# Kernel optimization log

Measured on AMD Instinct MI355X. Metric: run time of the kernel, lower is better.

## Reference

```python
import jax, jax.numpy as jnp
import numpy as np

STUDENT_FRAMES = [0, 2, 4, 6]
EXTRA_FRAMES = [1, 3, 5, 7]       # teacher-only frames, sorted
SHARED_T = [2, 4, 6]              # shared frames in teacher indexing
SHARED_S = [1, 2, 3]              # same frames in student indexing
TOPK = 4
EPS = 1e-8                        # eps of _cos_angle's F.normalize
HUBER_DELTA = 1.0
A1 = A2 = A3 = 1.0


def _huber(pred, target, delta=HUBER_DELTA):
    err = pred - target
    ae = jnp.abs(err)
    return jnp.where(ae <= delta, 0.5 * err * err, delta * (ae - 0.5 * delta))


def _angles(h, r, c):
    """Cosine angles for the triangle (shared=h [B,F,S,D], ref=r [B,R,D], sim=c [B,R,K,D]).
    Expands cos(a-b, c-b) via pairwise dot products so no [.,.,.,.,D] tensor is materialized.
    Returns (a1, a2, a3) each of shape [B,F,R,S,K]."""
    ss = jnp.einsum('bfsd,brkd->bfrsk', h, c)   # shared . sim
    sr = jnp.einsum('bfsd,brd->bfrs', h, r)     # shared . ref
    rk = jnp.einsum('brd,brkd->brk', r, c)      # ref . sim
    rr = jnp.sum(r * r, -1)                     # [B,R]
    kk = jnp.sum(c * c, -1)                     # [B,R,K]
    hh = jnp.sum(h * h, -1)                     # [B,F,S]
    sr_ = sr[..., None]                         # bfrs1
    rk_ = rk[:, None, :, None, :]               # b1r1k
    rr_ = rr[:, None, :, None, None]            # b1r11
    kk_ = kk[:, None, :, None, :]               # b1r1k
    hh_ = hh[:, :, None, :, None]               # bf1s1
    n_hr = jnp.sqrt(jnp.maximum(hh_ + rr_ - 2.0 * sr_, 0.0))  # ||shared-ref||
    n_cr = jnp.sqrt(jnp.maximum(kk_ + rr_ - 2.0 * rk_, 0.0))  # ||sim-ref||
    n_hc = jnp.sqrt(jnp.maximum(hh_ + kk_ - 2.0 * ss, 0.0))   # ||shared-sim||
    def cos(num, na, nb):
        return num / (jnp.maximum(na, EPS) * jnp.maximum(nb, EPS))
    a1 = cos(ss - sr_ - rk_ + rr_, n_hr, n_cr)  # cos(shared-ref, sim-ref)
    a2 = cos(sr_ - rk_ - ss + kk_, n_cr, n_hc)  # cos(ref-sim, shared-sim)
    a3 = cos(rk_ - sr_ - ss + hh_, n_hr, n_hc)  # cos(ref-shared, sim-shared)
    return a1, a2, a3


def setup_inputs() -> dict:
    key = jax.random.key(0)
    k1, k2, k3, k4 = jax.random.split(key, 4)
    B, V, P, D = 4, 8, 1369, 2048
    teacher_feats = jax.random.normal(k1, (B, V, P, D), jnp.float32)
    student_feats = jax.random.normal(k2, (B, len(STUDENT_FRAMES), P, D), jnp.float32)
    ref_perm = jax.random.permutation(k3, P)[:128].astype(jnp.int32)
    shared_perm = jax.random.permutation(k4, P)[:128].astype(jnp.int32)
    return {'teacher_feats': teacher_feats, 'student_feats': student_feats,
            'ref_perm': ref_perm, 'shared_perm': shared_perm}


def reference(teacher_feats, student_feats, ref_perm, shared_perm):
    teacher = jax.lax.stop_gradient(teacher_feats)  # teacher side is fully detached
    B, V, P, D = teacher.shape

    ref_t = teacher[:, STUDENT_FRAMES[0], ref_perm, :]        # [B,R,D]
    ref_s = student_feats[:, 0, ref_perm, :]                  # [B,R,D]

    # extra (teacher-only) frames concatenated along patches -> [B, 4*P, D]
    extra_t = teacher[:, jnp.array(EXTRA_FRAMES)].reshape(B, len(EXTRA_FRAMES) * P, D)

    # cosine similarity + topk selection (selection_mode='topk')
    ref_tn = ref_t / jnp.maximum(jnp.linalg.norm(ref_t, axis=-1, keepdims=True), 1e-12)
    extra_tn = extra_t / jnp.maximum(jnp.linalg.norm(extra_t, axis=-1, keepdims=True), 1e-12)
    sim = jnp.einsum('brd,bed->bre', ref_tn, extra_tn)        # [B,R,4P]
    _, idx = jax.lax.top_k(sim, TOPK)                         # [B,R,K]
    sim_high = jax.vmap(lambda e, i: e[i])(extra_t, idx)      # [B,R,K,D]

    shared_t = teacher[:, jnp.array(SHARED_T)][:, :, shared_perm, :]        # [B,F,S,D]
    shared_s = student_feats[:, jnp.array(SHARED_S)][:, :, shared_perm, :]  # [B,F,S,D]

    a1_t, a2_t, a3_t = _angles(shared_t, ref_t, sim_high)
    a1_s, a2_s, a3_s = _angles(shared_s, ref_s, sim_high)

    l1 = _huber(a1_s, a1_t).mean()
    l2 = _huber(a2_s, a2_t).mean()
    l3 = _huber(a3_s, a3_t).mean()
    loss = A1 * l1 + A2 * l2 + A3 * l3
    return loss
```

## Files before the change

### kernel.cpp

```cpp
#include <hip/hip_runtime.h>
#include <hip/hip_bf16.h>

#define B_ 4
#define V_ 8
#define P_ 1369
#define D_ 2048
#define R_ 128
#define F_ 3
#define K_ 4
#define E_ 5476
#define CAND_ 8
#define EPS_ 1e-8f
#define ETILES_ 86
#define SIMBLK_ (ETILES_*B_*2)
#define HOFF_ ((size_t)B_*384*640)

typedef unsigned short u16;
typedef __attribute__((ext_vector_type(8))) short bf16x8;
typedef __attribute__((ext_vector_type(4))) float f32x4;

__device__ inline int pack2bf(float lo, float hi){
  __hip_bfloat162 h = __float22bfloat162_rn(make_float2(lo, hi));
  int r; __builtin_memcpy(&r, &h, 4); return r;
}
__device__ inline float sq8(float4 a, float4 b){
  return a.x*a.x + a.y*a.y + a.z*a.z + a.w*a.w
       + b.x*b.x + b.y*b.y + b.z*b.z + b.w*b.w;
}
__device__ inline float huber1(float e){
  float ae = fabsf(e);
  return ae <= 1.0f ? 0.5f*e*e : (ae - 0.5f);
}
__device__ inline float blk_sum(float v, float* scr){
  for (int off = 32; off; off >>= 1) v += __shfl_xor(v, off, 64);
  __syncthreads();
  if ((threadIdx.x & 63) == 0) scr[threadIdx.x >> 6] = v;
  __syncthreads();
  float s = scr[0] + scr[1] + scr[2] + scr[3];
  __syncthreads();
  return s;
}

__global__ __launch_bounds__(256) void k_prep_ref(
    const float* __restrict__ teacher, const float* __restrict__ student,
    const int* __restrict__ ref_perm,
    u16* __restrict__ ref_tn, float* __restrict__ rr_t, float* __restrict__ rr_s){
  __shared__ float scr[4];
  int br = blockIdx.x, b = br >> 7, r = br & 127, t = threadIdx.x;
  int p = ref_perm[r];
  const float* tp = teacher + ((size_t)(b*V_)*P_ + p)*D_;
  const float* sp = student + ((size_t)(b*4)*P_ + p)*D_;
  float4 x0 = *(const float4*)(tp + t*8);
  float4 x1 = *(const float4*)(tp + t*8 + 4);
  float sumt = blk_sum(sq8(x0, x1), scr);
  float4 y0 = *(const float4*)(sp + t*8);
  float4 y1 = *(const float4*)(sp + t*8 + 4);
  float sums = blk_sum(sq8(y0, y1), scr);
  if (t == 0){ rr_t[br] = sumt; rr_s[br] = sums; }
  float inv = 1.0f / fmaxf(sqrtf(sumt), 1e-12f);
  int4 pt = { pack2bf(x0.x*inv, x0.y*inv), pack2bf(x0.z*inv, x0.w*inv),
              pack2bf(x1.x*inv, x1.y*inv), pack2bf(x1.z*inv, x1.w*inv) };
  *(int4*)(ref_tn + (size_t)br*D_ + t*8) = pt;
}

__global__ __launch_bounds__(256) void k_sim_fused(
    const float* __restrict__ teacher, const float* __restrict__ student,
    const u16* __restrict__ ref_tn, const int* __restrict__ shared_perm,
    float* __restrict__ simPart, float* __restrict__ nsqPart,
    u16* __restrict__ shT, u16* __restrict__ shS,
    float* __restrict__ hhT, float* __restrict__ hhS){
  __shared__ __align__(16) u16 As[128][72];
  __shared__ __align__(16) u16 Bs[64][72];
  __shared__ float scr4[4];
  int bx = blockIdx.x, t = threadIdx.x;
  if (bx < SIMBLK_){
    int h = bx / (ETILES_*B_);
    int rem = bx % (ETILES_*B_);
    int b = rem / ETILES_, et = rem % ETILES_;
    int e0 = et * 64;
    int lane = t & 63, w = t >> 6, wm = w >> 1, wn = w & 1;
    f32x4 acc[4][2];
    for (int i = 0; i < 4; i++)
      for (int j = 0; j < 2; j++)
        acc[i][j] = (f32x4){0.f, 0.f, 0.f, 0.f};
    int arow = t >> 1, acol = (t & 1) * 32;
    int brow = t >> 2, bcol = (t & 3) * 16;
    int e = e0 + brow;
    const u16* asrc = ref_tn + ((size_t)(b*128 + arow))*D_ + acol;
    const float* bsrc = nullptr;
    if (e < E_) bsrc = teacher + ((size_t)(b*V_ + 1 + 2*(e / P_))*P_ + (e % P_))*D_ + bcol;
    float q = 0.0f;
    int lr = lane & 15;
    int kbeg = h * 1024, kend = kbeg + 1024;
    int4 aa0, aa1, aa2, aa3;
    float4 za0, za1, za2, za3;
    {
      aa0 = *(const int4*)(asrc + kbeg);      aa1 = *(const int4*)(asrc + kbeg + 8);
      aa2 = *(const int4*)(asrc + kbeg + 16); aa3 = *(const int4*)(asrc + kbeg + 24);
      if (bsrc){
        za0 = *(const float4*)(bsrc + kbeg);      za1 = *(const float4*)(bsrc + kbeg + 4);
        za2 = *(const float4*)(bsrc + kbeg + 8);  za3 = *(const float4*)(bsrc + kbeg + 12);
      } else { za0 = make_float4(0.f,0.f,0.f,0.f); za1 = za0; za2 = za0; za3 = za0; }
    }
    for (int k0 = kbeg; k0 < kend; k0 += 64){
      __syncthreads();
      *(int4*)&As[arow][acol]      = aa0;
      *(int4*)&As[arow][acol + 8]  = aa1;
      *(int4*)&As[arow][acol + 16] = aa2;
      *(int4*)&As[arow][acol + 24] = aa3;
      q += sq8(za0, za1) + sq8(za2, za3);
      int4 p0 = { pack2bf(za0.x, za0.y), pack2bf(za0.z, za0.w),
                  pack2bf(za1.x, za1.y), pack2bf(za1.z, za1.w) };
      int4 p1 = { pack2bf(za2.x, za2.y), pack2bf(za2.z, za2.w),
                  pack2bf(za3.x, za3.y), pack2bf(za3.z, za3.w) };
      *(int4*)&Bs[brow][bcol]     = p0;
      *(int4*)&Bs[brow][bcol + 8] = p1;
      __syncthreads();
      int kn = k0 + 64;
      if (kn < kend){
        aa0 = *(const int4*)(asrc + kn);      aa1 = *(const int4*)(asrc + kn + 8);
        aa2 = *(const int4*)(asrc + kn + 16); aa3 = *(const int4*)(asrc + kn + 24);
        if (bsrc){
          za0 = *(const float4*)(bsrc + kn);      za1 = *(const float4*)(bsrc + kn + 4);
          za2 = *(const float4*)(bsrc + kn + 8);  za3 = *(const float4*)(bsrc + kn + 12);
        }
      }
#pragma unroll
      for (int kk = 0; kk < 2; kk++){
        int kof = kk*32 + (lane >> 4) * 8;
        bf16x8 bf0 = *(const bf16x8*)&Bs[wn*32 + lr][kof];
        bf16x8 bf1 = *(const bf16x8*)&Bs[wn*32 + 16 + lr][kof];
#pragma unroll
        for (int mi = 0; mi < 4; mi++){
          bf16x8 af = *(const bf16x8*)&As[wm*64 + mi*16 + lr][kof];
          acc[mi][0] = __builtin_amdgcn_mfma_f32_16x16x32_bf16(af, bf0, acc[mi][0], 0, 0, 0);
          acc[mi][1] = __builtin_amdgcn_mfma_f32_16x16x32_bf16(af, bf1, acc[mi][1], 0, 0, 0);
        }
      }
    }
    q += __shfl_xor(q, 1, 64);
    q += __shfl_xor(q, 2, 64);
    if ((t & 3) == 0 && e < E_) nsqPart[(size_t)(h*4 + b)*E_ + e] = q;
    int lg = lane >> 4;
#pragma unroll
    for (int mi = 0; mi < 4; mi++){
#pragma unroll
      for (int ni = 0; ni < 2; ni++){
        int el = wn*32 + ni*16 + lr;
        int e_idx = e0 + el;
        if (e_idx < E_){
#pragma unroll
          for (int reg = 0; reg < 4; reg++){
            int r_idx = wm*64 + mi*16 + lg*4 + reg;
            simPart[((size_t)((h*4 + b)*128 + r_idx))*E_ + e_idx] = acc[mi][ni][reg];
          }
        }
      }
    }
  } else {
    int id = bx - SIMBLK_;
    int b = id / 384, fs = id % 384;
    int f = fs >> 7, s = fs & 127;
    int p = shared_perm[s];
    const float* tp = teacher + ((size_t)(b*V_ + 2 + 2*f)*P_ + p)*D_;
    const float* sp = student + ((size_t)(b*4 + 1 + f)*P_ + p)*D_;
    float4 x0 = *(const float4*)(tp + t*8);
    float4 x1 = *(const float4*)(tp + t*8 + 4);
    float sumt = blk_sum(sq8(x0, x1), scr4);
    int4 pt = { pack2bf(x0.x, x0.y), pack2bf(x0.z, x0.w),
                pack2bf(x1.x, x1.y), pack2bf(x1.z, x1.w) };
    *(int4*)(shT + (size_t)id*D_ + t*8) = pt;
    float4 y0 = *(const float4*)(sp + t*8);
    float4 y1 = *(const float4*)(sp + t*8 + 4);
    float sums = blk_sum(sq8(y0, y1), scr4);
    int4 ps = { pack2bf(y0.x, y0.y), pack2bf(y0.z, y0.w),
                pack2bf(y1.x, y1.y), pack2bf(y1.z, y1.w) };
    *(int4*)(shS + (size_t)id*D_ + t*8) = ps;
    if (t == 0){ hhT[id] = sumt; hhS[id] = sums; }
  }
}

__global__ __launch_bounds__(256) void k_rescore(
    const float* __restrict__ teacher, const float* __restrict__ student,
    const int* __restrict__ ref_perm,
    const float* __restrict__ simPart, const float* __restrict__ nsqPart,
    const float* __restrict__ rr_t,
    u16* __restrict__ packT, u16* __restrict__ packS,
    float* __restrict__ kkw, float* __restrict__ rkT, float* __restrict__ rkS){
  __shared__ float v[E_];
  __shared__ float rT[D_];
  __shared__ float rS[D_];
  __shared__ float tv[256];
  __shared__ int   ti[256];
  __shared__ float rv[4];
  __shared__ int ri[4];
  __shared__ int cand[CAND_];
  __shared__ float csim[CAND_], cq[CAND_], cdT[CAND_];
  __shared__ int order[4];
  int br = blockIdx.x, b = br >> 7, r = br & 127, t = threadIdx.x;
  int lane = t & 63, w = t >> 6;
  const float* p0 = simPart + ((size_t)(b*128 + r))*E_;
  const float* p1 = simPart + ((size_t)((4 + b)*128 + r))*E_;
  const float* q0 = nsqPart + (size_t)b*E_;
  const float* q1 = nsqPart + (size_t)(4 + b)*E_;
  for (int i = t; i < E_; i += 256){
    float qq = q0[i] + q1[i];
    float inv = 1.0f / fmaxf(sqrtf(qq), 1e-12f);
    v[i] = (p0[i] + p1[i]) * inv;
  }
  __syncthreads();
  {
    float bv = -3.4e38f; int bi = 0x7fffffff;
    for (int i = t; i < E_; i += 256){
      float x = v[i];
      if (x > bv){ bv = x; bi = i; }
    }
    tv[t] = bv; ti[t] = bi;
  }
  __syncthreads();
  for (int c = 0; c < CAND_; c++){
    float mv = tv[t]; int mi2 = ti[t];
    for (int off = 32; off; off >>= 1){
      float ov = __shfl_down(mv, off, 64);
      int   oi = __shfl_down(mi2, off, 64);
      if (ov > mv || (ov == mv && oi < mi2)){ mv = ov; mi2 = oi; }
    }
    if (lane == 0){ rv[w] = mv; ri[w] = mi2; }
    __syncthreads();
    if (t == 0){
      for (int w2 = 1; w2 < 4; w2++)
        if (rv[w2] > rv[0] || (rv[w2] == rv[0] && ri[w2] < ri[0])){ rv[0] = rv[w2]; ri[0] = ri[w2]; }
      cand[c] = ri[0];
      v[ri[0]] = -3.4e38f;
    }
    __syncthreads();
    int win = cand[c];
    if (t == (win & 255)){
      float nb = -3.4e38f; int nbi = 0x7fffffff;
      for (int i = t; i < E_; i += 256){
        float x = v[i];
        if (x > nb){ nb = x; nbi = i; }
      }
      tv[t] = nb; ti[t] = nbi;
    }
    __syncthreads();
  }
  int p = ref_perm[r];
  const float* tp = teacher + ((size_t)(b*V_)*P_ + p)*D_;
  const float* sp = student + ((size_t)(b*4)*P_ + p)*D_;
  float4 x0 = *(const float4*)(tp + t*8);
  float4 x1 = *(const float4*)(tp + t*8 + 4);
  float4 y0 = *(const float4*)(sp + t*8);
  float4 y1 = *(const float4*)(sp + t*8 + 4);
  *(float4*)&rT[t*8]   = x0; *(float4*)&rT[t*8+4] = x1;
  *(float4*)&rS[t*8]   = y0; *(float4*)&rS[t*8+4] = y1;
  {
    int4 pt = { pack2bf(x0.x, x0.y), pack2bf(x0.z, x0.w),
                pack2bf(x1.x, x1.y), pack2bf(x1.z, x1.w) };
    *(int4*)(packT + ((size_t)(br*5 + 4))*D_ + t*8) = pt;
    int4 ps = { pack2bf(y0.x, y0.y), pack2bf(y0.z, y0.w),
                pack2bf(y1.x, y1.y), pack2bf(y1.z, y1.w) };
    *(int4*)(packS + ((size_t)(br*5 + 4))*D_ + t*8) = ps;
  }
  float invt = 1.0f / fmaxf(sqrtf(rr_t[br]), 1e-12f);
  __syncthreads();
  for (int c = w; c < CAND_; c += 4){
    int e = cand[c];
    const float* xp = teacher + ((size_t)(b*V_ + 1 + 2*(e / P_))*P_ + (e % P_))*D_;
    float d = 0.f, q = 0.f;
#pragma unroll
    for (int j = 0; j < 32; j++){
      float xv = xp[lane + 64*j];
      d += xv * rT[lane + 64*j];
      q += xv * xv;
    }
    for (int off = 32; off; off >>= 1){
      d += __shfl_xor(d, off, 64);
      q += __shfl_xor(q, off, 64);
    }
    if (lane == 0){
      cdT[c] = d; cq[c] = q;
      csim[c] = d * invt / fmaxf(sqrtf(q), 1e-12f);
    }
  }
  __syncthreads();
  if (t == 0){
    unsigned used = 0;
    for (int k = 0; k < 4; k++){
      int best = -1;
      for (int c = 0; c < CAND_; c++){
        if (used & (1u << c)) continue;
        if (best < 0){ best = c; continue; }
        if (csim[c] > csim[best] ||
            (csim[c] == csim[best] && cand[c] < cand[best])) best = c;
      }
      used |= 1u << best;
      order[k] = best;
    }
  }
  __syncthreads();
  {
    int c = order[w];
    int e = cand[c];
    const float* xp = teacher + ((size_t)(b*V_ + 1 + 2*(e / P_))*P_ + (e % P_))*D_;
    float ds = 0.f;
#pragma unroll
    for (int j = 0; j < 32; j++)
      ds += xp[lane + 64*j] * rS[lane + 64*j];
    for (int off = 32; off; off >>= 1) ds += __shfl_xor(ds, off, 64);
    if (lane == 0){
      kkw[br*4 + w] = cq[c];
      rkT[br*4 + w] = cdT[c];
      rkS[br*4 + w] = ds;
    }
    const float* src = xp + lane*32;
#pragma unroll
    for (int u = 0; u < 4; u++){
      float4 a  = *(const float4*)(src + u*8);
      float4 b2 = *(const float4*)(src + u*8 + 4);
      int4 pc = { pack2bf(a.x, a.y), pack2bf(a.z, a.w),
                  pack2bf(b2.x, b2.y), pack2bf(b2.z, b2.w) };
      size_t po = ((size_t)(br*5 + w))*D_ + lane*32 + u*8;
      *(int4*)(packT + po) = pc;
      *(int4*)(packS + po) = pc;
    }
  }
}

__global__ __launch_bounds__(256) void k_angle_gemm(
    const u16* __restrict__ shT, const u16* __restrict__ shS,
    const u16* __restrict__ packT, const u16* __restrict__ packS,
    float* __restrict__ outT, float* __restrict__ outS){
  __shared__ __align__(16) u16 As[128][72];
  __shared__ __align__(16) u16 Bs[64][72];
  int which = blockIdx.z >> 1, h = blockIdx.z & 1;
  const u16* A  = which ? shS : shT;
  const u16* Bp = which ? packS : packT;
  float* out = (which ? outS : outT) + h * HOFF_;
  int b = blockIdx.y;
  int mt = blockIdx.x % 3, nt = blockIdx.x / 3;
  int m0 = mt*128, n0 = nt*64;
  int t = threadIdx.x, lane = t & 63, w = t >> 6, wm = w >> 1, wn = w & 1;
  f32x4 acc[4][2];
  for (int i = 0; i < 4; i++)
    for (int j = 0; j < 2; j++)
      acc[i][j] = (f32x4){0.f, 0.f, 0.f, 0.f};
  int arow = t >> 1, acol = (t & 1) * 32;
  int brow = t >> 2, bcol = (t & 3) * 16;
  const u16* asrc = A  + ((size_t)(b*384 + m0 + arow))*D_ + acol;
  const u16* bsrc = Bp + ((size_t)(b*640 + n0 + brow))*D_ + bcol;
  int lr = lane & 15;
  int kbeg = h * 1024, kend = kbeg + 1024;
  int4 ra0, ra1, ra2, ra3, rb0, rb1;
  ra0 = *(const int4*)(asrc + kbeg);      ra1 = *(const int4*)(asrc + kbeg + 8);
  ra2 = *(const int4*)(asrc + kbeg + 16); ra3 = *(const int4*)(asrc + kbeg + 24);
  rb0 = *(const int4*)(bsrc + kbeg);      rb1 = *(const int4*)(bsrc + kbeg + 8);
  for (int k0 = kbeg; k0 < kend; k0 += 64){
    __syncthreads();
    *(int4*)&As[arow][acol]      = ra0;
    *(int4*)&As[arow][acol + 8]  = ra1;
    *(int4*)&As[arow][acol + 16] = ra2;
    *(int4*)&As[arow][acol + 24] = ra3;
    *(int4*)&Bs[brow][bcol]     = rb0;
    *(int4*)&Bs[brow][bcol + 8] = rb1;
    __syncthreads();
    int kn = k0 + 64;
    if (kn < kend){
      ra0 = *(const int4*)(asrc + kn);      ra1 = *(const int4*)(asrc + kn + 8);
      ra2 = *(const int4*)(asrc + kn + 16); ra3 = *(const int4*)(asrc + kn + 24);
      rb0 = *(const int4*)(bsrc + kn);      rb1 = *(const int4*)(bsrc + kn + 8);
    }
#pragma unroll
    for (int kk = 0; kk < 2; kk++){
      int kof = kk*32 + (lane >> 4) * 8;
      bf16x8 bf0 = *(const bf16x8*)&Bs[wn*32 + lr][kof];
      bf16x8 bf1 = *(const bf16x8*)&Bs[wn*32 + 16 + lr][kof];
#pragma unroll
      for (int mi = 0; mi < 4; mi++){
        bf16x8 af = *(const bf16x8*)&As[wm*64 + mi*16 + lr][kof];
        acc[mi][0] = __builtin_amdgcn_mfma_f32_16x16x32_bf16(af, bf0, acc[mi][0], 0, 0, 0);
        acc[mi][1] = __builtin_amdgcn_mfma_f32_16x16x32_bf16(af, bf1, acc[mi][1], 0, 0, 0);
      }
    }
  }
  int lg = lane >> 4;
#pragma unroll
  for (int mi = 0; mi < 4; mi++)
#pragma unroll
    for (int ni = 0; ni < 2; ni++)
#pragma unroll
      for (int reg = 0; reg < 4; reg++){
        int r_idx = wm*64 + mi*16 + lg*4 + reg;
        int c_idx = wn*32 + ni*16 + lr;
        out[((size_t)(b*384 + m0 + r_idx))*640 + n0 + c_idx] = acc[mi][ni][reg];
      }
}

__global__ __launch_bounds__(256) void k_assemble(
    const float* __restrict__ outT, const float* __restrict__ outS,
    const float* __restrict__ hhT, const float* __restrict__ hhS,
    const float* __restrict__ rrT, const float* __restrict__ rrS,
    const float* __restrict__ kkw, const float* __restrict__ rkT, const float* __restrict__ rkS,
    double* __restrict__ partials){
  __shared__ double dscr[4];
  int idx = blockIdx.x*256 + threadIdx.x;
  int r = idx & 127, s = (idx >> 7) & 127, bf = idx >> 14;
  int f = bf % 3, b = bf / 3;
  int fs = f*128 + s;
  size_t base = ((size_t)(b*384 + fs))*640 + r*5;
  const float* oT0 = outT + base; const float* oT1 = oT0 + HOFF_;
  const float* oS0 = outS + base; const float* oS1 = oS0 + HOFF_;
  float hh_t = hhT[b*384 + fs], hh_s = hhS[b*384 + fs];
  float rr_tv = rrT[b*128 + r], rr_sv = rrS[b*128 + r];
  float sr_t = oT0[4] + oT1[4], sr_s = oS0[4] + oS1[4];
  float nhr_t = sqrtf(fmaxf(hh_t + rr_tv - 2.0f*sr_t, 0.0f));
  float nhr_s = sqrtf(fmaxf(hh_s + rr_sv - 2.0f*sr_s, 0.0f));
  float h1 = 0.f, h2 = 0.f, h3 = 0.f;
#pragma unroll
  for (int k = 0; k < 4; k++){
    float ss_t = oT0[k] + oT1[k], ss_s = oS0[k] + oS1[k];
    float kk = kkw[(b*128 + r)*4 + k];
    float rk_t = rkT[(b*128 + r)*4 + k];
    float rk_s = rkS[(b*128 + r)*4 + k];
    float ncr_t = sqrtf(fmaxf(kk + rr_tv - 2.0f*rk_t, 0.0f));
    float ncr_s = sqrtf(fmaxf(kk + rr_sv - 2.0f*rk_s, 0.0f));
    float nhc_t = sqrtf(fmaxf(hh_t + kk - 2.0f*ss_t, 0.0f));
    float nhc_s = sqrtf(fmaxf(hh_s + kk - 2.0f*ss_s, 0.0f));
    float a1t = (ss_t - sr_t - rk_t + rr_tv) / (fmaxf(nhr_t, EPS_) * fmaxf(ncr_t, EPS_));
    float a2t = (sr_t - rk_t - ss_t + kk)    / (fmaxf(ncr_t, EPS_) * fmaxf(nhc_t, EPS_));
    float a3t = (rk_t - sr_t - ss_t + hh_t)  / (fmaxf(nhr_t, EPS_) * fmaxf(nhc_t, EPS_));
    float a1s = (ss_s - sr_s - rk_s + rr_sv) / (fmaxf(nhr_s, EPS_) * fmaxf(ncr_s, EPS_));
    float a2s = (sr_s - rk_s - ss_s + kk)    / (fmaxf(ncr_s, EPS_) * fmaxf(nhc_s, EPS_));
    float a3s = (rk_s - sr_s - ss_s + hh_s)  / (fmaxf(nhr_s, EPS_) * fmaxf(nhc_s, EPS_));
    h1 += huber1(a1s - a1t);
    h2 += huber1(a2s - a2t);
    h3 += huber1(a3s - a3t);
  }
  double d1 = h1, d2 = h2, d3 = h3;
  for (int off = 32; off; off >>= 1){
    d1 += __shfl_xor(d1, off, 64);
    d2 += __shfl_xor(d2, off, 64);
    d3 += __shfl_xor(d3, off, 64);
  }
  int w = threadIdx.x >> 6;
  if ((threadIdx.x & 63) == 0) dscr[w] = d1;
  __syncthreads();
  if (threadIdx.x == 0) partials[blockIdx.x*3 + 0] = dscr[0]+dscr[1]+dscr[2]+dscr[3];
  __syncthreads();
  if ((threadIdx.x & 63) == 0) dscr[w] = d2;
  __syncthreads();
  if (threadIdx.x == 0) partials[blockIdx.x*3 + 1] = dscr[0]+dscr[1]+dscr[2]+dscr[3];
  __syncthreads();
  if ((threadIdx.x & 63) == 0) dscr[w] = d3;
  __syncthreads();
  if (threadIdx.x == 0) partials[blockIdx.x*3 + 2] = dscr[0]+dscr[1]+dscr[2]+dscr[3];
}

__global__ __launch_bounds__(256) void k_final(
    const double* __restrict__ partials, float* __restrict__ out){
  __shared__ double dscr[12];
  int t = threadIdx.x;
  double l1 = 0, l2 = 0, l3 = 0;
  for (int i = t; i < 768; i += 256){
    l1 += partials[i*3 + 0];
    l2 += partials[i*3 + 1];
    l3 += partials[i*3 + 2];
  }
  for (int off = 32; off; off >>= 1){
    l1 += __shfl_xor(l1, off, 64);
    l2 += __shfl_xor(l2, off, 64);
    l3 += __shfl_xor(l3, off, 64);
  }
  int w = t >> 6;
  if ((t & 63) == 0){ dscr[w*3] = l1; dscr[w*3+1] = l2; dscr[w*3+2] = l3; }
  __syncthreads();
  if (t == 0){
    double L1 = dscr[0] + dscr[3] + dscr[6] + dscr[9];
    double L2 = dscr[1] + dscr[4] + dscr[7] + dscr[10];
    double L3 = dscr[2] + dscr[5] + dscr[8] + dscr[11];
    out[0] = (float)((L1 + L2 + L3) / 786432.0);
  }
}

extern "C" void kernel_launch(void* const* d_in, const int* in_sizes, int n_in,
                              void* d_out, int out_size, void* d_ws, size_t ws_size,
                              hipStream_t stream){
  (void)in_sizes; (void)n_in; (void)out_size; (void)ws_size;
  const float* teacher = (const float*)d_in[0];
  const float* student = (const float*)d_in[1];
  const int* ref_perm = (const int*)d_in[2];
  const int* shared_perm = (const int*)d_in[3];
  float* out = (float*)d_out;

  char* ws = (char*)d_ws;
  size_t off = 0;
  auto alloc = [&](size_t bytes)->char*{
    char* pp = ws + off;
    off += (bytes + 255) & ~(size_t)255;
    return pp;
  };
  u16*    ref_tn  = (u16*)   alloc((size_t)B_*R_*D_*sizeof(u16));
  float*  rr_t    = (float*) alloc(B_*R_*sizeof(float));
  float*  rr_s    = (float*) alloc(B_*R_*sizeof(float));
  float*  kkw     = (float*) alloc(B_*R_*K_*sizeof(float));
  float*  rkT     = (float*) alloc(B_*R_*K_*sizeof(float));
  float*  rkS     = (float*) alloc(B_*R_*K_*sizeof(float));
  u16*    shT     = (u16*)   alloc((size_t)B_*384*D_*sizeof(u16));
  u16*    shS     = (u16*)   alloc((size_t)B_*384*D_*sizeof(u16));
  float*  hhT     = (float*) alloc(B_*384*sizeof(float));
  float*  hhS     = (float*) alloc(B_*384*sizeof(float));
  float*  outT    = (float*) alloc((size_t)2*B_*384*640*sizeof(float));
  float*  outS    = (float*) alloc((size_t)2*B_*384*640*sizeof(float));
  double* partials= (double*)alloc(768*3*sizeof(double));
  float*  simPart = (float*) alloc((size_t)2*B_*R_*E_*sizeof(float));
  float*  nsqPart = (float*) alloc((size_t)2*B_*E_*sizeof(float));
  u16*    packT   = (u16*)   alloc((size_t)B_*R_*5*D_*sizeof(u16));
  u16*    packS   = (u16*)   alloc((size_t)B_*R_*5*D_*sizeof(u16));

  k_prep_ref<<<dim3(B_*R_), dim3(256), 0, stream>>>(teacher, student, ref_perm,
                                                    ref_tn, rr_t, rr_s);
  k_sim_fused<<<dim3(SIMBLK_ + 1536), dim3(256), 0, stream>>>(
      teacher, student, ref_tn, shared_perm, simPart, nsqPart, shT, shS, hhT, hhS);
  k_rescore<<<dim3(B_*R_), dim3(256), 0, stream>>>(teacher, student, ref_perm,
                                                   simPart, nsqPart, rr_t,
                                                   packT, packS, kkw, rkT, rkS);
  k_angle_gemm<<<dim3(30, B_, 4), dim3(256), 0, stream>>>(shT, shS, packT, packS, outT, outS);
  k_assemble<<<dim3(768), dim3(256), 0, stream>>>(outT, outS, hhT, hhS, rr_t, rr_s, kkw, rkT, rkS, partials);
  k_final<<<dim3(1), dim3(256), 0, stream>>>(partials, out);
}
```

Measured before the change: 126.4 us.

## Store split-K GEMM partials in bf16 and fuse final reduction via atomic counter

The split-K partial outputs of the similarity GEMM and the angle GEMM are now stored as bf16 instead of fp32. This halves the intermediate traffic between kernels. The separate final-reduction kernel is removed: the last assemble block, found through an atomic counter reset in the first kernel, sums the partials, which saves one launch. The bf16 partials lose precision, which could change top-k selection and the angle values near degeneracies.

```diff
diff --git a/kernel.cpp b/kernel.cpp
--- a/kernel.cpp
+++ b/kernel.cpp
@@ -14,11 +14,20 @@
 #define ETILES_ 86
 #define SIMBLK_ (ETILES_*B_*2)
 #define HOFF_ ((size_t)B_*384*640)
+#define NASM_ 768
 
 typedef unsigned short u16;
 typedef __attribute__((ext_vector_type(8))) short bf16x8;
 typedef __attribute__((ext_vector_type(4))) float f32x4;
 
+__device__ inline u16 f2bf(float f){
+  unsigned int u = __float_as_uint(f);
+  u = u + 0x7fffu + ((u >> 16) & 1u);
+  return (u16)(u >> 16);
+}
+__device__ inline float bf2f(u16 h){
+  return __uint_as_float((unsigned)h << 16);
+}
 __device__ inline int pack2bf(float lo, float hi){
   __hip_bfloat162 h = __float22bfloat162_rn(make_float2(lo, hi));
   int r; __builtin_memcpy(&r, &h, 4); return r;
@@ -44,9 +53,11 @@
 __global__ __launch_bounds__(256) void k_prep_ref(
     const float* __restrict__ teacher, const float* __restrict__ student,
     const int* __restrict__ ref_perm,
-    u16* __restrict__ ref_tn, float* __restrict__ rr_t, float* __restrict__ rr_s){
+    u16* __restrict__ ref_tn, float* __restrict__ rr_t, float* __restrict__ rr_s,
+    unsigned* __restrict__ cnt){
   __shared__ float scr[4];
   int br = blockIdx.x, b = br >> 7, r = br & 127, t = threadIdx.x;
+  if (br == 0 && t == 0) *cnt = 0u;
   int p = ref_perm[r];
   const float* tp = teacher + ((size_t)(b*V_)*P_ + p)*D_;
   const float* sp = student + ((size_t)(b*4)*P_ + p)*D_;
@@ -66,7 +77,7 @@
 __global__ __launch_bounds__(256) void k_sim_fused(
     const float* __restrict__ teacher, const float* __restrict__ student,
     const u16* __restrict__ ref_tn, const int* __restrict__ shared_perm,
-    float* __restrict__ simPart, float* __restrict__ nsqPart,
+    u16* __restrict__ simPart, float* __restrict__ nsqPart,
     u16* __restrict__ shT, u16* __restrict__ shS,
     float* __restrict__ hhT, float* __restrict__ hhS){
   __shared__ __align__(16) u16 As[128][72];
@@ -152,7 +163,7 @@
 #pragma unroll
           for (int reg = 0; reg < 4; reg++){
             int r_idx = wm*64 + mi*16 + lg*4 + reg;
-            simPart[((size_t)((h*4 + b)*128 + r_idx))*E_ + e_idx] = acc[mi][ni][reg];
+            simPart[((size_t)((h*4 + b)*128 + r_idx))*E_ + e_idx] = f2bf(acc[mi][ni][reg]);
           }
         }
       }
@@ -183,7 +194,7 @@
 __global__ __launch_bounds__(256) void k_rescore(
     const float* __restrict__ teacher, const float* __restrict__ student,
     const int* __restrict__ ref_perm,
-    const float* __restrict__ simPart, const float* __restrict__ nsqPart,
+    const u16* __restrict__ simPart, const float* __restrict__ nsqPart,
     const float* __restrict__ rr_t,
     u16* __restrict__ packT, u16* __restrict__ packS,
     float* __restrict__ kkw, float* __restrict__ rkT, float* __restrict__ rkS){
@@ -199,14 +210,14 @@
   __shared__ int order[4];
   int br = blockIdx.x, b = br >> 7, r = br & 127, t = threadIdx.x;
   int lane = t & 63, w = t >> 6;
-  const float* p0 = simPart + ((size_t)(b*128 + r))*E_;
-  const float* p1 = simPart + ((size_t)((4 + b)*128 + r))*E_;
+  const u16* p0 = simPart + ((size_t)(b*128 + r))*E_;
+  const u16* p1 = simPart + ((size_t)((4 + b)*128 + r))*E_;
   const float* q0 = nsqPart + (size_t)b*E_;
   const float* q1 = nsqPart + (size_t)(4 + b)*E_;
   for (int i = t; i < E_; i += 256){
     float qq = q0[i] + q1[i];
     float inv = 1.0f / fmaxf(sqrtf(qq), 1e-12f);
-    v[i] = (p0[i] + p1[i]) * inv;
+    v[i] = (bf2f(p0[i]) + bf2f(p1[i])) * inv;
   }
   __syncthreads();
   {
@@ -330,13 +341,13 @@
 __global__ __launch_bounds__(256) void k_angle_gemm(
     const u16* __restrict__ shT, const u16* __restrict__ shS,
     const u16* __restrict__ packT, const u16* __restrict__ packS,
-    float* __restrict__ outT, float* __restrict__ outS){
+    u16* __restrict__ outT, u16* __restrict__ outS){
   __shared__ __align__(16) u16 As[128][72];
   __shared__ __align__(16) u16 Bs[64][72];
   int which = blockIdx.z >> 1, h = blockIdx.z & 1;
   const u16* A  = which ? shS : shT;
   const u16* Bp = which ? packS : packT;
-  float* out = (which ? outS : outT) + h * HOFF_;
+  u16* out = (which ? outS : outT) + h * HOFF_;
   int b = blockIdx.y;
   int mt = blockIdx.x % 3, nt = blockIdx.x / 3;
   int m0 = mt*128, n0 = nt*64;
@@ -392,33 +403,36 @@
       for (int reg = 0; reg < 4; reg++){
         int r_idx = wm*64 + mi*16 + lg*4 + reg;
         int c_idx = wn*32 + ni*16 + lr;
-        out[((size_t)(b*384 + m0 + r_idx))*640 + n0 + c_idx] = acc[mi][ni][reg];
+        out[((size_t)(b*384 + m0 + r_idx))*640 + n0 + c_idx] = f2bf(acc[mi][ni][reg]);
       }
 }
 
 __global__ __launch_bounds__(256) void k_assemble(
-    const float* __restrict__ outT, const float* __restrict__ outS,
+    const u16* __restrict__ outT, const u16* __restrict__ outS,
     const float* __restrict__ hhT, const float* __restrict__ hhS,
     const float* __restrict__ rrT, const float* __restrict__ rrS,
     const float* __restrict__ kkw, const float* __restrict__ rkT, const float* __restrict__ rkS,
-    double* __restrict__ partials){
+    double* __restrict__ partials, unsigned* __restrict__ cnt, float* __restrict__ outF){
   __shared__ double dscr[4];
+  __shared__ double dfin[12];
+  __shared__ int lastFlag;
   int idx = blockIdx.x*256 + threadIdx.x;
   int r = idx & 127, s = (idx >> 7) & 127, bf = idx >> 14;
   int f = bf % 3, b = bf / 3;
   int fs = f*128 + s;
   size_t base = ((size_t)(b*384 + fs))*640 + r*5;
-  const float* oT0 = outT + base; const float* oT1 = oT0 + HOFF_;
-  const float* oS0 = outS + base; const float* oS1 = oS0 + HOFF_;
+  const u16* oT0 = outT + base; const u16* oT1 = oT0 + HOFF_;
+  const u16* oS0 = outS + base; const u16* oS1 = oS0 + HOFF_;
   float hh_t = hhT[b*384 + fs], hh_s = hhS[b*384 + fs];
   float rr_tv = rrT[b*128 + r], rr_sv = rrS[b*128 + r];
-  float sr_t = oT0[4] + oT1[4], sr_s = oS0[4] + oS1[4];
+  float sr_t = bf2f(oT0[4]) + bf2f(oT1[4]), sr_s = bf2f(oS0[4]) + bf2f(oS1[4]);
   float nhr_t = sqrtf(fmaxf(hh_t + rr_tv - 2.0f*sr_t, 0.0f));
   float nhr_s = sqrtf(fmaxf(hh_s + rr_sv - 2.0f*sr_s, 0.0f));
   float h1 = 0.f, h2 = 0.f, h3 = 0.f;
 #pragma unroll
   for (int k = 0; k < 4; k++){
-    float ss_t = oT0[k] + oT1[k], ss_s = oS0[k] + oS1[k];
+    float ss_t = bf2f(oT0[k]) + bf2f(oT1[k]);
+    float ss_s = bf2f(oS0[k]) + bf2f(oS1[k]);
     float kk = kkw[(b*128 + r)*4 + k];
     float rk_t = rkT[(b*128 + r)*4 + k];
     float rk_s = rkS[(b*128 + r)*4 + k];
@@ -453,32 +467,35 @@
   __syncthreads();
   if ((threadIdx.x & 63) == 0) dscr[w] = d3;
   __syncthreads();
-  if (threadIdx.x == 0) partials[blockIdx.x*3 + 2] = dscr[0]+dscr[1]+dscr[2]+dscr[3];
-}
-
-__global__ __launch_bounds__(256) void k_final(
-    const double* __restrict__ partials, float* __restrict__ out){
-  __shared__ double dscr[12];
-  int t = threadIdx.x;
-  double l1 = 0, l2 = 0, l3 = 0;
-  for (int i = t; i < 768; i += 256){
-    l1 += partials[i*3 + 0];
-    l2 += partials[i*3 + 1];
-    l3 += partials[i*3 + 2];
-  }
-  for (int off = 32; off; off >>= 1){
-    l1 += __shfl_xor(l1, off, 64);
-    l2 += __shfl_xor(l2, off, 64);
-    l3 += __shfl_xor(l3, off, 64);
-  }
-  int w = t >> 6;
-  if ((t & 63) == 0){ dscr[w*3] = l1; dscr[w*3+1] = l2; dscr[w*3+2] = l3; }
-  __syncthreads();
-  if (t == 0){
-    double L1 = dscr[0] + dscr[3] + dscr[6] + dscr[9];
-    double L2 = dscr[1] + dscr[4] + dscr[7] + dscr[10];
-    double L3 = dscr[2] + dscr[5] + dscr[8] + dscr[11];
-    out[0] = (float)((L1 + L2 + L3) / 786432.0);
+  if (threadIdx.x == 0){
+    partials[blockIdx.x*3 + 2] = dscr[0]+dscr[1]+dscr[2]+dscr[3];
+    __threadfence();
+    unsigned old = atomicAdd(cnt, 1u);
+    lastFlag = (old == NASM_ - 1) ? 1 : 0;
+  }
+  __syncthreads();
+  if (lastFlag){
+    __threadfence();
+    int t = threadIdx.x;
+    double l1 = 0, l2 = 0, l3 = 0;
+    for (int i = t; i < NASM_; i += 256){
+      l1 += partials[i*3 + 0];
+      l2 += partials[i*3 + 1];
+      l3 += partials[i*3 + 2];
+    }
+    for (int off = 32; off; off >>= 1){
+      l1 += __shfl_xor(l1, off, 64);
+      l2 += __shfl_xor(l2, off, 64);
+      l3 += __shfl_xor(l3, off, 64);
+    }
+    if ((t & 63) == 0){ dfin[w*3] = l1; dfin[w*3+1] = l2; dfin[w*3+2] = l3; }
+    __syncthreads();
+    if (t == 0){
+      double L1 = dfin[0] + dfin[3] + dfin[6] + dfin[9];
+      double L2 = dfin[1] + dfin[4] + dfin[7] + dfin[10];
+      double L3 = dfin[2] + dfin[5] + dfin[8] + dfin[11];
+      outF[0] = (float)((L1 + L2 + L3) / 786432.0);
+    }
   }
 }
 
@@ -509,22 +526,23 @@
   u16*    shS     = (u16*)   alloc((size_t)B_*384*D_*sizeof(u16));
   float*  hhT     = (float*) alloc(B_*384*sizeof(float));
   float*  hhS     = (float*) alloc(B_*384*sizeof(float));
-  float*  outT    = (float*) alloc((size_t)2*B_*384*640*sizeof(float));
-  float*  outS    = (float*) alloc((size_t)2*B_*384*640*sizeof(float));
-  double* partials= (double*)alloc(768*3*sizeof(double));
-  float*  simPart = (float*) alloc((size_t)2*B_*R_*E_*sizeof(float));
+  u16*    outT    = (u16*)   alloc((size_t)2*B_*384*640*sizeof(u16));
+  u16*    outS    = (u16*)   alloc((size_t)2*B_*384*640*sizeof(u16));
+  double* partials= (double*)alloc(NASM_*3*sizeof(double));
+  unsigned* cnt   = (unsigned*)alloc(256);
+  u16*    simPart = (u16*)   alloc((size_t)2*B_*R_*E_*sizeof(u16));
   float*  nsqPart = (float*) alloc((size_t)2*B_*E_*sizeof(float));
   u16*    packT   = (u16*)   alloc((size_t)B_*R_*5*D_*sizeof(u16));
   u16*    packS   = (u16*)   alloc((size_t)B_*R_*5*D_*sizeof(u16));
 
   k_prep_ref<<<dim3(B_*R_), dim3(256), 0, stream>>>(teacher, student, ref_perm,
-                                                    ref_tn, rr_t, rr_s);
+                                                    ref_tn, rr_t, rr_s, cnt);
   k_sim_fused<<<dim3(SIMBLK_ + 1536), dim3(256), 0, stream>>>(
       teacher, student, ref_tn, shared_perm, simPart, nsqPart, shT, shS, hhT, hhS);
   k_rescore<<<dim3(B_*R_), dim3(256), 0, stream>>>(teacher, student, ref_perm,
                                                    simPart, nsqPart, rr_t,
                                                    packT, packS, kkw, rkT, rkS);
   k_angle_gemm<<<dim3(30, B_, 4), dim3(256), 0, stream>>>(shT, shS, packT, packS, outT, outS);
-  k_assemble<<<dim3(768), dim3(256), 0, stream>>>(outT, outS, hhT, hhS, rr_t, rr_s, kkw, rkT, rkS, partials);
-  k_final<<<dim3(1), dim3(256), 0, stream>>>(partials, out);
-}
+  k_assemble<<<dim3(NASM_), dim3(256), 0, stream>>>(outT, outS, hhT, hhS, rr_t, rr_s,
+                                                    kkw, rkT, rkS, partials, cnt, out);
+}
```

New measurement: 132.1 us. 1.05x slower.

## Widen sim GEMM E-tile to 128 and split K three ways

Applied to the files above, without the earlier changes.

The similarity GEMM tile grows from 128x64 to 128x128 along the extra-patch dimension, so each ref_tn A tile is reused across twice as many columns and each wave issues 16 MFMAs per k-step instead of 8. The K split changes from two halves of 1024 to three chunks (704/704/640), which keeps the block count similar (516 vs 688). The rescore kernel now sums three partial sim and norm buffers. The cost is more accumulator registers and LDS per block, which may lower occupancy, plus an extra partial buffer to write and read.

```diff
diff --git a/kernel.cpp b/kernel.cpp
--- a/kernel.cpp
+++ b/kernel.cpp
@@ -11,8 +11,8 @@
 #define E_ 5476
 #define CAND_ 8
 #define EPS_ 1e-8f
-#define ETILES_ 86
-#define SIMBLK_ (ETILES_*B_*2)
+#define ETILES_ 43
+#define SIMBLK_ (ETILES_*B_*3)
 #define HOFF_ ((size_t)B_*384*640)
 
 typedef unsigned short u16;
@@ -70,51 +70,64 @@
     u16* __restrict__ shT, u16* __restrict__ shS,
     float* __restrict__ hhT, float* __restrict__ hhS){
   __shared__ __align__(16) u16 As[128][72];
-  __shared__ __align__(16) u16 Bs[64][72];
+  __shared__ __align__(16) u16 Bs[128][72];
   __shared__ float scr4[4];
   int bx = blockIdx.x, t = threadIdx.x;
   if (bx < SIMBLK_){
     int h = bx / (ETILES_*B_);
     int rem = bx % (ETILES_*B_);
     int b = rem / ETILES_, et = rem % ETILES_;
-    int e0 = et * 64;
+    int e0 = et * 128;
     int lane = t & 63, w = t >> 6, wm = w >> 1, wn = w & 1;
-    f32x4 acc[4][2];
+    f32x4 acc[4][4];
+#pragma unroll
     for (int i = 0; i < 4; i++)
-      for (int j = 0; j < 2; j++)
+#pragma unroll
+      for (int j = 0; j < 4; j++)
         acc[i][j] = (f32x4){0.f, 0.f, 0.f, 0.f};
-    int arow = t >> 1, acol = (t & 1) * 32;
-    int brow = t >> 2, bcol = (t & 3) * 16;
-    int e = e0 + brow;
-    const u16* asrc = ref_tn + ((size_t)(b*128 + arow))*D_ + acol;
+    int row = t >> 1, col32 = (t & 1) * 32;
+    int e = e0 + row;
+    const u16* asrc = ref_tn + ((size_t)(b*128 + row))*D_ + col32;
     const float* bsrc = nullptr;
-    if (e < E_) bsrc = teacher + ((size_t)(b*V_ + 1 + 2*(e / P_))*P_ + (e % P_))*D_ + bcol;
+    if (e < E_) bsrc = teacher + ((size_t)(b*V_ + 1 + 2*(e / P_))*P_ + (e % P_))*D_ + col32;
     float q = 0.0f;
     int lr = lane & 15;
-    int kbeg = h * 1024, kend = kbeg + 1024;
+    int kbeg = (h == 0) ? 0 : (h == 1 ? 704 : 1408);
+    int kend = (h == 0) ? 704 : (h == 1 ? 1408 : 2048);
     int4 aa0, aa1, aa2, aa3;
-    float4 za0, za1, za2, za3;
+    float4 za0, za1, za2, za3, za4, za5, za6, za7;
     {
       aa0 = *(const int4*)(asrc + kbeg);      aa1 = *(const int4*)(asrc + kbeg + 8);
       aa2 = *(const int4*)(asrc + kbeg + 16); aa3 = *(const int4*)(asrc + kbeg + 24);
       if (bsrc){
         za0 = *(const float4*)(bsrc + kbeg);      za1 = *(const float4*)(bsrc + kbeg + 4);
         za2 = *(const float4*)(bsrc + kbeg + 8);  za3 = *(const float4*)(bsrc + kbeg + 12);
-      } else { za0 = make_float4(0.f,0.f,0.f,0.f); za1 = za0; za2 = za0; za3 = za0; }
+        za4 = *(const float4*)(bsrc + kbeg + 16); za5 = *(const float4*)(bsrc + kbeg + 20);
+        za6 = *(const float4*)(bsrc + kbeg + 24); za7 = *(const float4*)(bsrc + kbeg + 28);
+      } else {
+        za0 = make_float4(0.f,0.f,0.f,0.f); za1 = za0; za2 = za0; za3 = za0;
+        za4 = za0; za5 = za0; za6 = za0; za7 = za0;
+      }
     }
     for (int k0 = kbeg; k0 < kend; k0 += 64){
       __syncthreads();
-      *(int4*)&As[arow][acol]      = aa0;
-      *(int4*)&As[arow][acol + 8]  = aa1;
-      *(int4*)&As[arow][acol + 16] = aa2;
-      *(int4*)&As[arow][acol + 24] = aa3;
-      q += sq8(za0, za1) + sq8(za2, za3);
+      *(int4*)&As[row][col32]      = aa0;
+      *(int4*)&As[row][col32 + 8]  = aa1;
+      *(int4*)&As[row][col32 + 16] = aa2;
+      *(int4*)&As[row][col32 + 24] = aa3;
+      q += sq8(za0, za1) + sq8(za2, za3) + sq8(za4, za5) + sq8(za6, za7);
       int4 p0 = { pack2bf(za0.x, za0.y), pack2bf(za0.z, za0.w),
                   pack2bf(za1.x, za1.y), pack2bf(za1.z, za1.w) };
       int4 p1 = { pack2bf(za2.x, za2.y), pack2bf(za2.z, za2.w),
                   pack2bf(za3.x, za3.y), pack2bf(za3.z, za3.w) };
-      *(int4*)&Bs[brow][bcol]     = p0;
-      *(int4*)&Bs[brow][bcol + 8] = p1;
+      int4 p2 = { pack2bf(za4.x, za4.y), pack2bf(za4.z, za4.w),
+                  pack2bf(za5.x, za5.y), pack2bf(za5.z, za5.w) };
+      int4 p3 = { pack2bf(za6.x, za6.y), pack2bf(za6.z, za6.w),
+                  pack2bf(za7.x, za7.y), pack2bf(za7.z, za7.w) };
+      *(int4*)&Bs[row][col32]      = p0;
+      *(int4*)&Bs[row][col32 + 8]  = p1;
+      *(int4*)&Bs[row][col32 + 16] = p2;
+      *(int4*)&Bs[row][col32 + 24] = p3;
       __syncthreads();
       int kn = k0 + 64;
       if (kn < kend){
@@ -123,30 +136,34 @@
         if (bsrc){
           za0 = *(const float4*)(bsrc + kn);      za1 = *(const float4*)(bsrc + kn + 4);
           za2 = *(const float4*)(bsrc + kn + 8);  za3 = *(const float4*)(bsrc + kn + 12);
+          za4 = *(const float4*)(bsrc + kn + 16); za5 = *(const float4*)(bsrc + kn + 20);
+          za6 = *(const float4*)(bsrc + kn + 24); za7 = *(const float4*)(bsrc + kn + 28);
         }
       }
 #pragma unroll
       for (int kk = 0; kk < 2; kk++){
         int kof = kk*32 + (lane >> 4) * 8;
-        bf16x8 bf0 = *(const bf16x8*)&Bs[wn*32 + lr][kof];
-        bf16x8 bf1 = *(const bf16x8*)&Bs[wn*32 + 16 + lr][kof];
+        bf16x8 bf[4];
+#pragma unroll
+        for (int ni = 0; ni < 4; ni++)
+          bf[ni] = *(const bf16x8*)&Bs[wn*64 + ni*16 + lr][kof];
 #pragma unroll
         for (int mi = 0; mi < 4; mi++){
           bf16x8 af = *(const bf16x8*)&As[wm*64 + mi*16 + lr][kof];
-          acc[mi][0] = __builtin_amdgcn_mfma_f32_16x16x32_bf16(af, bf0, acc[mi][0], 0, 0, 0);
-          acc[mi][1] = __builtin_amdgcn_mfma_f32_16x16x32_bf16(af, bf1, acc[mi][1], 0, 0, 0);
+#pragma unroll
+          for (int ni = 0; ni < 4; ni++)
+            acc[mi][ni] = __builtin_amdgcn_mfma_f32_16x16x32_bf16(af, bf[ni], acc[mi][ni], 0, 0, 0);
         }
       }
     }
     q += __shfl_xor(q, 1, 64);
-    q += __shfl_xor(q, 2, 64);
-    if ((t & 3) == 0 && e < E_) nsqPart[(size_t)(h*4 + b)*E_ + e] = q;
+    if ((t & 1) == 0 && e < E_) nsqPart[(size_t)(h*4 + b)*E_ + e] = q;
     int lg = lane >> 4;
 #pragma unroll
     for (int mi = 0; mi < 4; mi++){
 #pragma unroll
-      for (int ni = 0; ni < 2; ni++){
-        int el = wn*32 + ni*16 + lr;
+      for (int ni = 0; ni < 4; ni++){
+        int el = wn*64 + ni*16 + lr;
         int e_idx = e0 + el;
         if (e_idx < E_){
 #pragma unroll
@@ -201,12 +218,14 @@
   int lane = t & 63, w = t >> 6;
   const float* p0 = simPart + ((size_t)(b*128 + r))*E_;
   const float* p1 = simPart + ((size_t)((4 + b)*128 + r))*E_;
+  const float* p2 = simPart + ((size_t)((8 + b)*128 + r))*E_;
   const float* q0 = nsqPart + (size_t)b*E_;
   const float* q1 = nsqPart + (size_t)(4 + b)*E_;
+  const float* q2 = nsqPart + (size_t)(8 + b)*E_;
   for (int i = t; i < E_; i += 256){
-    float qq = q0[i] + q1[i];
+    float qq = q0[i] + q1[i] + q2[i];
     float inv = 1.0f / fmaxf(sqrtf(qq), 1e-12f);
-    v[i] = (p0[i] + p1[i]) * inv;
+    v[i] = (p0[i] + p1[i] + p2[i]) * inv;
   }
   __syncthreads();
   {
@@ -512,8 +531,8 @@
   float*  outT    = (float*) alloc((size_t)2*B_*384*640*sizeof(float));
   float*  outS    = (float*) alloc((size_t)2*B_*384*640*sizeof(float));
   double* partials= (double*)alloc(768*3*sizeof(double));
-  float*  simPart = (float*) alloc((size_t)2*B_*R_*E_*sizeof(float));
-  float*  nsqPart = (float*) alloc((size_t)2*B_*E_*sizeof(float));
+  float*  simPart = (float*) alloc((size_t)3*B_*R_*E_*sizeof(float));
+  float*  nsqPart = (float*) alloc((size_t)3*B_*E_*sizeof(float));
   u16*    packT   = (u16*)   alloc((size_t)B_*R_*5*D_*sizeof(u16));
   u16*    packS   = (u16*)   alloc((size_t)B_*R_*5*D_*sizeof(u16));
 
@@ -525,6 +544,7 @@
                                                    simPart, nsqPart, rr_t,
                                                    packT, packS, kkw, rkT, rkS);
   k_angle_gemm<<<dim3(30, B_, 4), dim3(256), 0, stream>>>(shT, shS, packT, packS, outT, outS);
-  k_assemble<<<dim3(768), dim3(256), 0, stream>>>(outT, outS, hhT, hhS, rr_t, rr_s, kkw, rkT, rkS, partials);
+  k_assemble<<<dim3(768), dim3(256), 0, stream>>>(outT, outS, hhT, hhS, rr_t, rr_s,
+                                                  kkw, rkT, rkS, partials);
   k_final<<<dim3(1), dim3(256), 0, stream>>>(partials, out);
 }
```

New measurement: 143.1 us. +13.3%, slower.
